# Kernel optimization log

Measured on AMD Instinct MI355X. Metric: run time of the kernel, lower is better.

The kernel has to match this reference:

```python
import jax, jax.numpy as jnp
import numpy as np

D_QUERY = 512
D_AUDIO = 512
D_OUT = 512
B, HW, S = 16, 4096, 1024


def setup_inputs() -> dict:
    key = jax.random.key(0)
    ks = jax.random.split(key, 8)
    sc_q = 1.0 / np.sqrt(D_QUERY)
    sc_a = 1.0 / np.sqrt(D_AUDIO)
    return {
        "x": jax.random.normal(ks[0], (B, HW, D_QUERY), dtype=jnp.float32),
        "audio_embed": jax.random.normal(ks[1], (B, S, D_AUDIO), dtype=jnp.float32),
        "Wq": jax.random.uniform(ks[2], (D_QUERY, D_OUT), jnp.float32, -sc_q, sc_q),
        "bq": jax.random.uniform(ks[3], (D_OUT,), jnp.float32, -sc_q, sc_q),
        "Wk": jax.random.uniform(ks[4], (D_AUDIO, D_OUT), jnp.float32, -sc_a, sc_a),
        "bk": jax.random.uniform(ks[5], (D_OUT,), jnp.float32, -sc_a, sc_a),
        "Wv": jax.random.uniform(ks[6], (D_AUDIO, D_OUT), jnp.float32, -sc_a, sc_a),
        "bv": jax.random.uniform(ks[7], (D_OUT,), jnp.float32, -sc_a, sc_a),
    }


def reference(x, audio_embed, Wq, bq, Wk, bk, Wv, bv):
    # Linear projections (nn.Linear: y = x @ W^T + b; we store W already transposed)
    Q = x @ Wq + bq                      # [B, HW, D_OUT]
    K = audio_embed @ Wk + bk            # [B, S, D_OUT]
    V = audio_embed @ Wv + bv            # [B, S, D_OUT]
    scale = 1.0 / (K.shape[-1] ** 0.5)   # divide by sqrt(d_out), per source
    scores = jnp.einsum("bnd,bsd->bns", Q, K) * scale  # [B, HW, S]
    attn = jax.nn.softmax(scores, axis=-1)
    return jnp.einsum("bns,bsd->bnd", attn, V)         # [B, HW, D_OUT]
```

## Files before the change

kernel.cpp:

```cpp
#include <hip/hip_runtime.h>
#include <hip/hip_bf16.h>

typedef __attribute__((ext_vector_type(8))) short bf16x8;
typedef __attribute__((ext_vector_type(4))) float f32x4;
typedef __attribute__((ext_vector_type(4))) unsigned short ushort4v;

__device__ __forceinline__ float bf_bits_to_f(short s) {
  unsigned int u = ((unsigned int)(unsigned short)s) << 16;
  union { unsigned int u; float f; } c; c.u = u; return c.f;
}
__device__ __forceinline__ unsigned short f_to_bf_bits(float f) {
  union { float f; unsigned int u; } c; c.f = f;
  unsigned int r = c.u + 0x7FFFu + ((c.u >> 16) & 1u);
  return (unsigned short)(r >> 16);
}

__global__ __launch_bounds__(256) void cvt_bf16_kernel(const float* __restrict__ in,
                                                       unsigned short* __restrict__ out,
                                                       long n) {
  const long nchunks = n >> 2;
  const long stride = (long)gridDim.x * 256;
  for (long c = (long)blockIdx.x * 256 + threadIdx.x; c < nchunks; c += stride) {
    f32x4 v = *(const f32x4*)(in + c * 4);
    ushort4v o;
    o[0] = f_to_bf_bits(v[0]); o[1] = f_to_bf_bits(v[1]);
    o[2] = f_to_bf_bits(v[2]); o[3] = f_to_bf_bits(v[3]);
    *(ushort4v*)(out + c * 4) = o;
  }
}

__global__ __launch_bounds__(256) void transpose_w_kernel(
    const float* __restrict__ W0, const float* __restrict__ W1, const float* __restrict__ W2,
    unsigned short* __restrict__ T0, unsigned short* __restrict__ T1, unsigned short* __restrict__ T2) {
  const float* W = (blockIdx.z == 0) ? W0 : (blockIdx.z == 1) ? W1 : W2;
  unsigned short* T = (blockIdx.z == 0) ? T0 : (blockIdx.z == 1) ? T1 : T2;
  __shared__ float t[32][33];
  const int tx = threadIdx.x & 31, ty = threadIdx.x >> 5;
  const int n0 = blockIdx.x * 32, k0 = blockIdx.y * 32;
#pragma unroll
  for (int j = 0; j < 4; ++j)
    t[ty + 8 * j][tx] = W[(long)(k0 + ty + 8 * j) * 512 + n0 + tx];
  __syncthreads();
#pragma unroll
  for (int j = 0; j < 4; ++j)
    T[(long)(n0 + ty + 8 * j) * 512 + k0 + tx] = f_to_bf_bits(t[tx][ty + 8 * j]);
}

template <bool BIAS, bool TRANSOUT, bool OUTBF16, bool EXPSTATS, bool AFP32, bool DIVSTATS>
__global__ __launch_bounds__(256) void gemm_kernel(
    const void* __restrict__ Aptr,
    const unsigned short* __restrict__ BT,
    const float* __restrict__ bias,
    void* __restrict__ Cout,
    const int K, const float scale,
    const long strideA, const long strideBT, const long strideC, const int ldc,
    const int nx, const int ny, float* __restrict__ stats) {
  __shared__ unsigned short lds[8192];
  __shared__ float ssum[128][2];
  __shared__ float invl[128];
  const int nwg = gridDim.x;
  const int chunk = nwg >> 3;
  const int bid = blockIdx.x;
  const int swz = (bid & 7) * chunk + (bid >> 3);
  const int bx = swz % nx;
  const int t1 = swz / nx;
  const int by = t1 % ny;
  const int bz = t1 / ny;

  const int tid = threadIdx.x;
  const int lane = tid & 63;
  const int wv = tid >> 6;
  const int wr = wv >> 1, wc = wv & 1;
  const unsigned short* Ab = (const unsigned short*)Aptr + (long)bz * strideA + (long)by * 128 * K;
  const float* Af = (const float*)Aptr + (long)bz * strideA + (long)by * 128 * K;
  const unsigned short* Bb = BT + (long)bz * strideBT + (long)bx * 128 * K;

  if (DIVSTATS) {
    if (tid < 128) {
      const long srow = (long)bz * 4096 + (long)by * 128 + tid;
      float l = 0.f;
#pragma unroll
      for (int cb = 0; cb < 8; ++cb) l += stats[srow * 8 + cb];
      invl[tid] = 1.f / l;
    }
  }

  f32x4 acc[4][4];
#pragma unroll
  for (int m = 0; m < 4; ++m)
#pragma unroll
    for (int n = 0; n < 4; ++n) acc[m][n] = (f32x4){0.f, 0.f, 0.f, 0.f};

  const int r15 = lane & 15, g = lane >> 4;
  const int kiters = K >> 5;

  int arow[2], acolb[2];
#pragma unroll
  for (int i = 0; i < 2; ++i) {
    const int c = i * 4 + wv;
    const int boff = c * 1024 + lane * 16;
    arow[i] = boff >> 6;
    acolb[i] = boff & 63;
  }
  f32x4 pa[2][2];
  if (AFP32) {
#pragma unroll
    for (int i = 0; i < 2; ++i) {
      const float* s = Af + (long)arow[i] * K + (acolb[i] >> 1);
      pa[i][0] = *(const f32x4*)s;
      pa[i][1] = *(const f32x4*)(s + 4);
    }
  }

  for (int kt = 0; kt < kiters; ++kt) {
#pragma unroll
    for (int i = 0; i < 2; ++i) {
      const int c = i * 4 + wv;
      const char* srcB = (const char*)Bb + (long)arow[i] * (K * 2) + kt * 64 + acolb[i];
      __builtin_amdgcn_global_load_lds(
          (const __attribute__((address_space(1))) void*)srcB,
          (__attribute__((address_space(3))) void*)(lds + 4096 + c * 512), 16, 0, 0);
      if (!AFP32) {
        const char* srcA = (const char*)Ab + (long)arow[i] * (K * 2) + kt * 64 + acolb[i];
        __builtin_amdgcn_global_load_lds(
            (const __attribute__((address_space(1))) void*)srcA,
            (__attribute__((address_space(3))) void*)(lds + c * 512), 16, 0, 0);
      }
    }
    if (AFP32) {
#pragma unroll
      for (int i = 0; i < 2; ++i) {
        const int c = i * 4 + wv;
        bf16x8 w;
#pragma unroll
        for (int e = 0; e < 4; ++e) {
          w[e] = (short)f_to_bf_bits(pa[i][0][e]);
          w[4 + e] = (short)f_to_bf_bits(pa[i][1][e]);
        }
        *(bf16x8*)&lds[c * 512 + lane * 8] = w;
      }
      if (kt < kiters - 1) {
#pragma unroll
        for (int i = 0; i < 2; ++i) {
          const float* s = Af + (long)arow[i] * K + (kt + 1) * 32 + (acolb[i] >> 1);
          pa[i][0] = *(const f32x4*)s;
          pa[i][1] = *(const f32x4*)(s + 4);
        }
      }
    }
    __syncthreads();

    bf16x8 af[4], bf[4];
#pragma unroll
    for (int m = 0; m < 4; ++m)
      af[m] = *(const bf16x8*)&lds[(wr * 64 + m * 16 + r15) * 32 + g * 8];
#pragma unroll
    for (int n = 0; n < 4; ++n)
      bf[n] = *(const bf16x8*)&lds[4096 + (wc * 64 + n * 16 + r15) * 32 + g * 8];
#pragma unroll
    for (int m = 0; m < 4; ++m)
#pragma unroll
      for (int n = 0; n < 4; ++n)
        acc[m][n] = __builtin_amdgcn_mfma_f32_16x16x32_bf16(af[m], bf[n], acc[m][n], 0, 0, 0);
    __syncthreads();
  }

  if (EXPSTATS) {
#pragma unroll
    for (int m = 0; m < 4; ++m)
#pragma unroll
      for (int n = 0; n < 4; ++n)
#pragma unroll
        for (int j = 0; j < 4; ++j) acc[m][n][j] = __expf(acc[m][n][j]);
#pragma unroll
    for (int m = 0; m < 4; ++m)
#pragma unroll
      for (int j = 0; j < 4; ++j) {
        float s = acc[m][0][j] + acc[m][1][j] + acc[m][2][j] + acc[m][3][j];
        s += __shfl_xor(s, 1);
        s += __shfl_xor(s, 2);
        s += __shfl_xor(s, 4);
        s += __shfl_xor(s, 8);
        if (r15 == 0) ssum[wr * 64 + m * 16 + g * 4 + j][wc] = s;
      }
    __syncthreads();
    if (r15 == 0 && wc == 0) {
#pragma unroll
      for (int m = 0; m < 4; ++m)
#pragma unroll
        for (int j = 0; j < 4; ++j) {
          const int rl = wr * 64 + m * 16 + g * 4 + j;
          stats[((long)bz * 4096 + (long)by * 128 + rl) * 8 + bx] = ssum[rl][0] + ssum[rl][1];
        }
    }
  }

  const long crow0 = (long)by * 128 + wr * 64;
  const long ccol0 = (long)bx * 128 + wc * 64;
#pragma unroll
  for (int n = 0; n < 4; ++n) {
    const long col = ccol0 + n * 16 + r15;
    const float bv = BIAS ? bias[col] : 0.f;
#pragma unroll
    for (int m = 0; m < 4; ++m) {
      const f32x4 v = acc[m][n];
#pragma unroll
      for (int j = 0; j < 4; ++j) {
        const int rl = wr * 64 + m * 16 + g * 4 + j;
        const long row = crow0 + m * 16 + g * 4 + j;
        const float rowscale = DIVSTATS ? invl[rl] : scale;
        const float val = (v[j] + bv) * rowscale;
        const long idx = TRANSOUT ? (col * (long)ldc + row) : (row * (long)ldc + col);
        if (OUTBF16)
          ((unsigned short*)Cout + (long)bz * strideC)[idx] = f_to_bf_bits(val);
        else
          ((float*)Cout + (long)bz * strideC)[idx] = val;
      }
    }
  }
}

extern "C" void kernel_launch(void* const* d_in, const int* in_sizes, int n_in,
                              void* d_out, int out_size, void* d_ws, size_t ws_size,
                              hipStream_t stream) {
  (void)in_sizes; (void)n_in; (void)out_size; (void)ws_size;
  const float* x     = (const float*)d_in[0];
  const float* audio = (const float*)d_in[1];
  const float* Wq    = (const float*)d_in[2];
  const float* bq    = (const float*)d_in[3];
  const float* Wk    = (const float*)d_in[4];
  const float* bk    = (const float*)d_in[5];
  const float* Wv    = (const float*)d_in[6];
  const float* bv    = (const float*)d_in[7];
  float* out = (float*)d_out;

  char* ws = (char*)d_ws;
  size_t off = 0;
  auto carve = [&](size_t bytes) { char* p = ws + off; off += (bytes + 255) & ~(size_t)255; return p; };
  unsigned short* ab  = (unsigned short*)carve((size_t)16384 * 512 * 2);
  unsigned short* wqt = (unsigned short*)carve((size_t)512 * 512 * 2);
  unsigned short* wkt = (unsigned short*)carve((size_t)512 * 512 * 2);
  unsigned short* wvt = (unsigned short*)carve((size_t)512 * 512 * 2);
  unsigned short* Qb  = (unsigned short*)carve((size_t)65536 * 512 * 2);
  unsigned short* Kb  = (unsigned short*)carve((size_t)16384 * 512 * 2);
  unsigned short* Vt  = (unsigned short*)carve((size_t)16384 * 512 * 2);
  unsigned short* Pb  = (unsigned short*)carve((size_t)65536 * 1024 * 2);
  float*          ls  = (float*)carve((size_t)65536 * 8 * 4);

  cvt_bf16_kernel<<<1024, 256, 0, stream>>>(audio, ab, (long)16384 * 512);
  transpose_w_kernel<<<dim3(16, 16, 3), 256, 0, stream>>>(Wq, Wk, Wv, wqt, wkt, wvt);
  gemm_kernel<true, false, true, false, true, false><<<4 * 512, 256, 0, stream>>>(
      x, wqt, bq, Qb, 512, 0.044194173824159216f, 0, 0, 0, 512, 4, 512, nullptr);
  gemm_kernel<true, false, true, false, false, false><<<4 * 128, 256, 0, stream>>>(
      ab, wkt, bk, Kb, 512, 1.f, 0, 0, 0, 512, 4, 128, nullptr);
  gemm_kernel<true, true, true, false, false, false><<<4 * 8 * 16, 256, 0, stream>>>(
      ab, wvt, bv, Vt, 512, 1.f, (long)1024 * 512, 0, (long)512 * 1024, 1024, 4, 8, nullptr);
  gemm_kernel<false, false, true, true, false, false><<<8 * 32 * 16, 256, 0, stream>>>(
      Qb, Kb, nullptr, Pb, 512, 1.f,
      (long)4096 * 512, (long)1024 * 512, (long)4096 * 1024, 1024, 8, 32, ls);
  gemm_kernel<false, false, false, false, false, true><<<4 * 32 * 16, 256, 0, stream>>>(
      Pb, Vt, nullptr, out, 1024, 1.f,
      (long)4096 * 1024, (long)512 * 1024, (long)4096 * 512, 512, 4, 32, ls);
}
```

Baseline: 403.9 us.

## Add 256x256 pipelined GEMM kernel for score and PV stages

Adds a new 512-thread GEMM kernel with 256x256 output tiles and a four-buffer LDS ring that prefetches three k-steps ahead using direct global-to-LDS loads and explicit vmcnt waits. The QK^T/exp and PV/normalize stages move onto it, so each row now has 4 partial row-sum stats instead of 8. The larger tiles are meant to raise data reuse per loaded byte, and the pipelining plus setprio are meant to hide memory latency behind MFMA. The cost is more registers and LDS per block (128 KB LDS with launch bounds of 2 blocks), which can reduce occupancy. The hand-written wait counts also depend on how the compiler orders the loads.

```diff
diff --git a/kernel.cpp b/kernel.cpp
--- a/kernel.cpp
+++ b/kernel.cpp
@@ -4,6 +4,9 @@
 typedef __attribute__((ext_vector_type(8))) short bf16x8;
 typedef __attribute__((ext_vector_type(4))) float f32x4;
 typedef __attribute__((ext_vector_type(4))) unsigned short ushort4v;
+
+#define AS1 __attribute__((address_space(1)))
+#define AS3 __attribute__((address_space(3)))
 
 __device__ __forceinline__ float bf_bits_to_f(short s) {
   unsigned int u = ((unsigned int)(unsigned short)s) << 16;
@@ -46,18 +49,16 @@
     T[(long)(n0 + ty + 8 * j) * 512 + k0 + tx] = f_to_bf_bits(t[tx][ty + 8 * j]);
 }
 
-template <bool BIAS, bool TRANSOUT, bool OUTBF16, bool EXPSTATS, bool AFP32, bool DIVSTATS>
+template <bool BIAS, bool TRANSOUT, bool AFP32>
 __global__ __launch_bounds__(256) void gemm_kernel(
     const void* __restrict__ Aptr,
     const unsigned short* __restrict__ BT,
     const float* __restrict__ bias,
-    void* __restrict__ Cout,
+    unsigned short* __restrict__ Cout,
     const int K, const float scale,
     const long strideA, const long strideBT, const long strideC, const int ldc,
-    const int nx, const int ny, float* __restrict__ stats) {
+    const int nx, const int ny) {
   __shared__ unsigned short lds[8192];
-  __shared__ float ssum[128][2];
-  __shared__ float invl[128];
   const int nwg = gridDim.x;
   const int chunk = nwg >> 3;
   const int bid = blockIdx.x;
@@ -75,16 +76,6 @@
   const float* Af = (const float*)Aptr + (long)bz * strideA + (long)by * 128 * K;
   const unsigned short* Bb = BT + (long)bz * strideBT + (long)bx * 128 * K;
 
-  if (DIVSTATS) {
-    if (tid < 128) {
-      const long srow = (long)bz * 4096 + (long)by * 128 + tid;
-      float l = 0.f;
-#pragma unroll
-      for (int cb = 0; cb < 8; ++cb) l += stats[srow * 8 + cb];
-      invl[tid] = 1.f / l;
-    }
-  }
-
   f32x4 acc[4][4];
 #pragma unroll
   for (int m = 0; m < 4; ++m)
@@ -118,13 +109,11 @@
       const int c = i * 4 + wv;
       const char* srcB = (const char*)Bb + (long)arow[i] * (K * 2) + kt * 64 + acolb[i];
       __builtin_amdgcn_global_load_lds(
-          (const __attribute__((address_space(1))) void*)srcB,
-          (__attribute__((address_space(3))) void*)(lds + 4096 + c * 512), 16, 0, 0);
+          (const AS1 void*)srcB, (AS3 void*)(lds + 4096 + c * 512), 16, 0, 0);
       if (!AFP32) {
         const char* srcA = (const char*)Ab + (long)arow[i] * (K * 2) + kt * 64 + acolb[i];
         __builtin_amdgcn_global_load_lds(
-            (const __attribute__((address_space(1))) void*)srcA,
-            (__attribute__((address_space(3))) void*)(lds + c * 512), 16, 0, 0);
+            (const AS1 void*)srcA, (AS3 void*)(lds + c * 512), 16, 0, 0);
       }
     }
     if (AFP32) {
@@ -165,15 +154,134 @@
     __syncthreads();
   }
 
+  const long crow0 = (long)by * 128 + wr * 64;
+  const long ccol0 = (long)bx * 128 + wc * 64;
+#pragma unroll
+  for (int n = 0; n < 4; ++n) {
+    const long col = ccol0 + n * 16 + r15;
+    const float bv = BIAS ? bias[col] : 0.f;
+#pragma unroll
+    for (int m = 0; m < 4; ++m) {
+      const f32x4 v = acc[m][n];
+#pragma unroll
+      for (int j = 0; j < 4; ++j) {
+        const long row = crow0 + m * 16 + g * 4 + j;
+        const float val = (v[j] + bv) * scale;
+        const long idx = TRANSOUT ? (col * (long)ldc + row) : (row * (long)ldc + col);
+        (Cout + (long)bz * strideC)[idx] = f_to_bf_bits(val);
+      }
+    }
+  }
+}
+
+template <bool EXPSTATS, bool DIVSTATS>
+__global__ __launch_bounds__(512, 2) void gemm256_kernel(
+    const unsigned short* __restrict__ A,
+    const unsigned short* __restrict__ BT,
+    void* __restrict__ Cout,
+    const int K,
+    const long strideA, const long strideBT, const long strideC, const int ldc,
+    const int nx, const int ny, float* __restrict__ stats) {
+  __shared__ __align__(16) char ldsb[4][32768];
+  __shared__ float ssum[256][4];
+  __shared__ float invl[256];
+
+  const int nwg = gridDim.x;
+  const int chunk = nwg >> 3;
+  const int bid = blockIdx.x;
+  const int swz = (bid & 7) * chunk + (bid >> 3);
+  const int bx = swz % nx;
+  const int t1 = swz / nx;
+  const int by = t1 % ny;
+  const int bz = t1 / ny;
+
+  const int tid = threadIdx.x;
+  const int lane = tid & 63;
+  const int w = tid >> 6;
+  const int wm = w >> 2, wn = w & 3;
+  const int r15 = lane & 15, g = lane >> 4;
+
+  const unsigned short* Ab = A + (long)bz * strideA + (long)by * 256 * K;
+  const unsigned short* Bb = BT + (long)bz * strideBT + (long)bx * 256 * K;
+  const int rowstride = K * 2;
+
+  if (DIVSTATS) {
+    if (tid < 256) {
+      const f32x4 s = *(const f32x4*)&stats[((long)bz * 4096 + (long)by * 256 + tid) * 4];
+      invl[tid] = 1.f / (s[0] + s[1] + s[2] + s[3]);
+    }
+  }
+
+  const int boff0 = tid * 16;
+  const int boff1 = 8192 + tid * 16;
+  const int arow0 = boff0 >> 6, acol0 = boff0 & 63;
+  const int arow1 = boff1 >> 6, acol1 = boff1 & 63;
+
+  auto stage = [&](int kt2, int bsel) {
+    char* dst = ldsb[bsel];
+    const char* sA = (const char*)Ab + kt2 * 64;
+    const char* sB = (const char*)Bb + kt2 * 64;
+    __builtin_amdgcn_global_load_lds((const AS1 void*)(sA + (long)arow0 * rowstride + acol0),
+                                     (AS3 void*)(dst + boff0), 16, 0, 0);
+    __builtin_amdgcn_global_load_lds((const AS1 void*)(sB + (long)arow0 * rowstride + acol0),
+                                     (AS3 void*)(dst + 16384 + boff0), 16, 0, 0);
+    __builtin_amdgcn_global_load_lds((const AS1 void*)(sA + (long)arow1 * rowstride + acol1),
+                                     (AS3 void*)(dst + boff1), 16, 0, 0);
+    __builtin_amdgcn_global_load_lds((const AS1 void*)(sB + (long)arow1 * rowstride + acol1),
+                                     (AS3 void*)(dst + 16384 + boff1), 16, 0, 0);
+  };
+
+  f32x4 acc[8][4];
+#pragma unroll
+  for (int m = 0; m < 8; ++m)
+#pragma unroll
+    for (int n = 0; n < 4; ++n) acc[m][n] = (f32x4){0.f, 0.f, 0.f, 0.f};
+
+  const int kiters = K >> 5;
+  stage(0, 0);
+  stage(1, 1);
+  stage(2, 2);
+
+  for (int kt = 0; kt < kiters; ++kt) {
+    if (kt < kiters - 2) {
+      asm volatile("s_waitcnt vmcnt(8)" ::: "memory");
+    } else if (kt == kiters - 2) {
+      asm volatile("s_waitcnt vmcnt(4)" ::: "memory");
+    } else {
+      asm volatile("s_waitcnt vmcnt(0)" ::: "memory");
+    }
+    __builtin_amdgcn_s_barrier();
+    __builtin_amdgcn_sched_barrier(0);
+    if (kt + 3 < kiters) stage(kt + 3, (kt + 3) & 3);
+
+    const char* bA = ldsb[kt & 3];
+    const char* bB = ldsb[kt & 3] + 16384;
+    bf16x8 af[8], bfr[4];
+#pragma unroll
+    for (int m = 0; m < 8; ++m)
+      af[m] = *(const bf16x8*)(bA + (wm * 128 + m * 16 + r15) * 64 + g * 16);
+#pragma unroll
+    for (int n = 0; n < 4; ++n)
+      bfr[n] = *(const bf16x8*)(bB + (wn * 64 + n * 16 + r15) * 64 + g * 16);
+
+    __builtin_amdgcn_s_setprio(1);
+#pragma unroll
+    for (int m = 0; m < 8; ++m)
+#pragma unroll
+      for (int n = 0; n < 4; ++n)
+        acc[m][n] = __builtin_amdgcn_mfma_f32_16x16x32_bf16(af[m], bfr[n], acc[m][n], 0, 0, 0);
+    __builtin_amdgcn_s_setprio(0);
+  }
+
   if (EXPSTATS) {
 #pragma unroll
-    for (int m = 0; m < 4; ++m)
+    for (int m = 0; m < 8; ++m)
 #pragma unroll
       for (int n = 0; n < 4; ++n)
 #pragma unroll
         for (int j = 0; j < 4; ++j) acc[m][n][j] = __expf(acc[m][n][j]);
 #pragma unroll
-    for (int m = 0; m < 4; ++m)
+    for (int m = 0; m < 8; ++m)
 #pragma unroll
       for (int j = 0; j < 4; ++j) {
         float s = acc[m][0][j] + acc[m][1][j] + acc[m][2][j] + acc[m][3][j];
@@ -181,43 +289,35 @@
         s += __shfl_xor(s, 2);
         s += __shfl_xor(s, 4);
         s += __shfl_xor(s, 8);
-        if (r15 == 0) ssum[wr * 64 + m * 16 + g * 4 + j][wc] = s;
+        if (r15 == 0) ssum[wm * 128 + m * 16 + g * 4 + j][wn] = s;
       }
     __syncthreads();
-    if (r15 == 0 && wc == 0) {
-#pragma unroll
-      for (int m = 0; m < 4; ++m)
-#pragma unroll
-        for (int j = 0; j < 4; ++j) {
-          const int rl = wr * 64 + m * 16 + g * 4 + j;
-          stats[((long)bz * 4096 + (long)by * 128 + rl) * 8 + bx] = ssum[rl][0] + ssum[rl][1];
+    if (tid < 256) {
+      const float t = ssum[tid][0] + ssum[tid][1] + ssum[tid][2] + ssum[tid][3];
+      stats[((long)bz * 4096 + (long)by * 256 + tid) * 4 + bx] = t;
+    }
+  }
+
+  const long crow0 = (long)by * 256 + wm * 128;
+  const long ccol0 = (long)bx * 256 + wn * 64;
+#pragma unroll
+  for (int m = 0; m < 8; ++m)
+#pragma unroll
+    for (int j = 0; j < 4; ++j) {
+      const int rl = wm * 128 + m * 16 + g * 4 + j;
+      const long row = crow0 + m * 16 + g * 4 + j;
+#pragma unroll
+      for (int n = 0; n < 4; ++n) {
+        const long col = ccol0 + n * 16 + r15;
+        if (EXPSTATS) {
+          ((unsigned short*)Cout + (long)bz * strideC)[row * (long)ldc + col] =
+              f_to_bf_bits(acc[m][n][j]);
+        } else {
+          const float sc = DIVSTATS ? invl[rl] : 1.f;
+          ((float*)Cout + (long)bz * strideC)[row * (long)ldc + col] = acc[m][n][j] * sc;
         }
-    }
-  }
-
-  const long crow0 = (long)by * 128 + wr * 64;
-  const long ccol0 = (long)bx * 128 + wc * 64;
-#pragma unroll
-  for (int n = 0; n < 4; ++n) {
-    const long col = ccol0 + n * 16 + r15;
-    const float bv = BIAS ? bias[col] : 0.f;
-#pragma unroll
-    for (int m = 0; m < 4; ++m) {
-      const f32x4 v = acc[m][n];
-#pragma unroll
-      for (int j = 0; j < 4; ++j) {
-        const int rl = wr * 64 + m * 16 + g * 4 + j;
-        const long row = crow0 + m * 16 + g * 4 + j;
-        const float rowscale = DIVSTATS ? invl[rl] : scale;
-        const float val = (v[j] + bv) * rowscale;
-        const long idx = TRANSOUT ? (col * (long)ldc + row) : (row * (long)ldc + col);
-        if (OUTBF16)
-          ((unsigned short*)Cout + (long)bz * strideC)[idx] = f_to_bf_bits(val);
-        else
-          ((float*)Cout + (long)bz * strideC)[idx] = val;
-      }
-    }
-  }
+      }
+    }
 }
 
 extern "C" void kernel_launch(void* const* d_in, const int* in_sizes, int n_in,
@@ -245,20 +345,20 @@
   unsigned short* Kb  = (unsigned short*)carve((size_t)16384 * 512 * 2);
   unsigned short* Vt  = (unsigned short*)carve((size_t)16384 * 512 * 2);
   unsigned short* Pb  = (unsigned short*)carve((size_t)65536 * 1024 * 2);
-  float*          ls  = (float*)carve((size_t)65536 * 8 * 4);
+  float*          ls  = (float*)carve((size_t)65536 * 4 * 4);
 
   cvt_bf16_kernel<<<1024, 256, 0, stream>>>(audio, ab, (long)16384 * 512);
   transpose_w_kernel<<<dim3(16, 16, 3), 256, 0, stream>>>(Wq, Wk, Wv, wqt, wkt, wvt);
-  gemm_kernel<true, false, true, false, true, false><<<4 * 512, 256, 0, stream>>>(
-      x, wqt, bq, Qb, 512, 0.044194173824159216f, 0, 0, 0, 512, 4, 512, nullptr);
-  gemm_kernel<true, false, true, false, false, false><<<4 * 128, 256, 0, stream>>>(
-      ab, wkt, bk, Kb, 512, 1.f, 0, 0, 0, 512, 4, 128, nullptr);
-  gemm_kernel<true, true, true, false, false, false><<<4 * 8 * 16, 256, 0, stream>>>(
-      ab, wvt, bv, Vt, 512, 1.f, (long)1024 * 512, 0, (long)512 * 1024, 1024, 4, 8, nullptr);
-  gemm_kernel<false, false, true, true, false, false><<<8 * 32 * 16, 256, 0, stream>>>(
-      Qb, Kb, nullptr, Pb, 512, 1.f,
-      (long)4096 * 512, (long)1024 * 512, (long)4096 * 1024, 1024, 8, 32, ls);
-  gemm_kernel<false, false, false, false, false, true><<<4 * 32 * 16, 256, 0, stream>>>(
-      Pb, Vt, nullptr, out, 1024, 1.f,
-      (long)4096 * 1024, (long)512 * 1024, (long)4096 * 512, 512, 4, 32, ls);
-}
+  gemm_kernel<true, false, true><<<4 * 512, 256, 0, stream>>>(
+      x, wqt, bq, Qb, 512, 0.044194173824159216f, 0, 0, 0, 512, 4, 512);
+  gemm_kernel<true, false, false><<<4 * 128, 256, 0, stream>>>(
+      ab, wkt, bk, Kb, 512, 1.f, 0, 0, 0, 512, 4, 128);
+  gemm_kernel<true, true, false><<<4 * 8 * 16, 256, 0, stream>>>(
+      ab, wvt, bv, Vt, 512, 1.f, (long)1024 * 512, 0, (long)512 * 1024, 1024, 4, 8);
+  gemm256_kernel<true, false><<<4 * 16 * 16, 512, 0, stream>>>(
+      Qb, Kb, Pb, 512,
+      (long)4096 * 512, (long)1024 * 512, (long)4096 * 1024, 1024, 4, 16, ls);
+  gemm256_kernel<false, true><<<2 * 16 * 16, 512, 0, stream>>>(
+      Pb, Vt, out, 1024,
+      (long)4096 * 1024, (long)512 * 1024, (long)4096 * 512, 512, 2, 16, ls);
+}
```

Result: faster. 378.9 us (-6.2%).
